# Optimization experiments

Hardware: AMD Instinct MI355X
Metric: run time of the kernel (lower is better)

The kernel has to match this reference:

```python
import jax, jax.numpy as jnp
import numpy as np

N, E = 2048, 262144
SDIM, VDIM, EDIM = 256, 64, 32
NUM_ATOM_FEATURES, NUM_BOND_TYPES, NMOL = 16, 5, 64


def setup_inputs() -> dict:
    key = jax.random.key(0)
    ks = jax.random.split(key, 18)
    def lin(k, fan_in, shape):
        return jax.random.uniform(k, shape, jnp.float32, -1.0, 1.0) / np.sqrt(fan_in)
    inp = {
        "s": jax.random.normal(ks[0], (N, SDIM), jnp.float32),
        "v": jax.random.normal(ks[1], (N, 3, VDIM), jnp.float32),
        "p": jax.random.normal(ks[2], (N, 3), jnp.float32),
        "e": jax.random.normal(ks[3], (E, EDIM), jnp.float32),
        "batch": jnp.sort(jax.random.randint(ks[4], (N,), 0, NMOL)),
        "edge_index_global": jax.random.randint(ks[5], (2, E), 0, N),
        # learned params (torch DenseLayer == Linear): W [in,out], b [out]
        "Ws": lin(ks[6], SDIM, (SDIM, SDIM)),   "bs": lin(ks[7], SDIM, (SDIM,)),
        "Wc": lin(ks[8], VDIM, (VDIM, 1)),                                      # coords_lin, no bias
        "Wa": lin(ks[9], SDIM, (SDIM, NUM_ATOM_FEATURES)), "ba": lin(ks[10], SDIM, (NUM_ATOM_FEATURES,)),
        "Wb": lin(ks[11], EDIM, (EDIM, SDIM)),  "bb": lin(ks[12], EDIM, (SDIM,)),
        "W0": lin(ks[13], SDIM + 1, (SDIM + 1, SDIM)), "b0": lin(ks[14], SDIM + 1, (SDIM,)),
        "W1": lin(ks[15], SDIM, (SDIM, NUM_BOND_TYPES)), "b1": lin(ks[16], SDIM, (NUM_BOND_TYPES,)),
    }
    return inp


def reference(s, v, p, e, batch, edge_index_global,
              Ws, bs, Wc, Wa, ba, Wb, bb, W0, b0, W1, b1):
    # shared scalar mapping with SiLU
    s_h = jax.nn.silu(s @ Ws + bs)                              # [N, SDIM]
    coords = (v @ Wc)[..., 0]                                   # [N,3,VDIM]@[VDIM,1] -> [N,3]
    atoms_pred = s_h @ Wa + ba                                  # [N, NUM_ATOM_FEATURES]

    j, i = edge_index_global[0], edge_index_global[1]
    # coords_param == 'data': add positions then remove per-graph mean (scatter_mean)
    coords_pred = p + coords
    sums = jax.ops.segment_sum(coords_pred, batch, num_segments=NMOL)       # [NMOL,3]
    cnts = jax.ops.segment_sum(jnp.ones((N, 1), s.dtype), batch, num_segments=NMOL)
    coords_pred = coords_pred - (sums / jnp.maximum(cnts, 1.0))[batch]

    d = jnp.sum((coords_pred[i] - coords_pred[j]) ** 2, axis=-1, keepdims=True)  # [E,1]

    # dense edge matrix construction + symmetrization (as in the original)
    e_dense = jnp.zeros((N, N, EDIM), e.dtype).at[j, i].set(e)  # [N,N,EDIM]
    e_dense = 0.5 * (e_dense + jnp.swapaxes(e_dense, 0, 1))
    e_sym = e_dense[j, i]                                        # [E,EDIM]

    f = s_h[i] + s_h[j] + (e_sym @ Wb + bb)                      # [E,SDIM]
    edge = jnp.concatenate([f, d], axis=-1)                      # [E,SDIM+1]
    bonds_pred = jax.nn.silu(edge @ W0 + b0) @ W1 + b1           # [E,NUM_BOND_TYPES]
    return coords_pred, atoms_pred, bonds_pred
```

## Files before the change

kernel.cpp:

```cpp
#include <hip/hip_runtime.h>
#include <hip/hip_bf16.h>

typedef __bf16 bf16_8 __attribute__((ext_vector_type(8)));
typedef __bf16 bf16_4 __attribute__((ext_vector_type(4)));
typedef float f32x4 __attribute__((ext_vector_type(4)));

__device__ __forceinline__ float silu_f(float x) {
    return x * __builtin_amdgcn_rcpf(1.0f + __expf(-x));
}

__device__ __forceinline__ unsigned hslot(unsigned cell, unsigned nslots) {
    return (unsigned)(((unsigned long long)(cell * 2654435761u) * nslots) >> 32);
}
__device__ __forceinline__ int map_lookup(unsigned nslots,
                                          const unsigned long long* __restrict__ H, unsigned cell) {
    unsigned slot = hslot(cell, nslots);
    for (int pr = 0; pr < 4096; pr++) {
        unsigned long long v = H[slot];
        if (v == 0ull) return -1;
        if ((unsigned)(v >> 32) == cell) return (int)(v & 0xFFFFFFFFu) - 1;
        slot++; if (slot == nslots) slot = 0;
    }
    return -1;
}

__global__ __launch_bounds__(256) void kS(float* __restrict__ out, int n, float val) {
    int i = blockIdx.x * 256 + threadIdx.x;
    if (i < n) out[i] = val;
}

__global__ __launch_bounds__(256) void kZ(f32x4* __restrict__ a, size_t na16,
                                          f32x4* __restrict__ b, size_t nb16) {
    size_t i = (size_t)blockIdx.x * 256 + threadIdx.x;
    size_t stride = (size_t)gridDim.x * 256;
    f32x4 z = {0.f, 0.f, 0.f, 0.f};
    for (size_t k = i; k < na16; k += stride) a[k] = z;
    for (size_t k = i; k < nb16; k += stride) b[k] = z;
}

__global__ __launch_bounds__(256, 4) void kP(
    const float* __restrict__ s, const float* __restrict__ Ws, const float* __restrict__ bs,
    const float* __restrict__ W0, const float* __restrict__ Wa, const float* __restrict__ ba,
    const float* __restrict__ v, const float* __restrict__ p,
    const float* __restrict__ Wc, const float* __restrict__ Wb, const float* __restrict__ bb,
    const float* __restrict__ b0, const float* __restrict__ W1,
    const int* __restrict__ batch, const int* __restrict__ ei,
    int N, int E, int gaB, int coordB, int mapB,
    unsigned nslots, unsigned long long* __restrict__ H,
    __bf16* __restrict__ G, __bf16* __restrict__ wqT, __bf16* __restrict__ w1Tg,
    float* __restrict__ w0L, float* __restrict__ b0p,
    float* __restrict__ cp, float* __restrict__ sums, float* __restrict__ cnts,
    float* __restrict__ outA)
{
    __shared__ __align__(16) char LDSC[37376];
    int b = blockIdx.x, t = threadIdx.x;

    if (b < gaB) {
        __bf16* s_bf  = (__bf16*)LDSC;
        __bf16* sh_bf = (__bf16*)(LDSC + 8448);
        __bf16* wT    = (__bf16*)(LDSC + 16896);
        int wv = t >> 6, lane = t & 63;
        int l16 = lane & 15, q8 = (lane >> 4) * 8, r4b = (lane >> 4) * 4;
        int r0 = b * 16;
        {
            int row = t >> 4, c0 = (t & 15) * 16;
            const float* sp = s + (long long)(r0 + row) * 256 + c0;
            bool ok = (r0 + row) < N;
            f32x4 a0 = ok ? *(const f32x4*)(sp + 0)  : (f32x4){0.f,0.f,0.f,0.f};
            f32x4 a1 = ok ? *(const f32x4*)(sp + 4)  : (f32x4){0.f,0.f,0.f,0.f};
            f32x4 a2 = ok ? *(const f32x4*)(sp + 8)  : (f32x4){0.f,0.f,0.f,0.f};
            f32x4 a3 = ok ? *(const f32x4*)(sp + 12) : (f32x4){0.f,0.f,0.f,0.f};
            bf16_8 p0, p1;
#pragma unroll
            for (int q = 0; q < 4; q++) {
                p0[q] = (__bf16)a0[q]; p0[q + 4] = (__bf16)a1[q];
                p1[q] = (__bf16)a2[q]; p1[q + 4] = (__bf16)a3[q];
            }
            *(bf16_8*)(s_bf + row * 264 + c0) = p0;
            *(bf16_8*)(s_bf + row * 264 + c0 + 8) = p1;
        }
        __syncthreads();
        __bf16* wTw = wT + wv * 2560;
        float ld[32];

        f32x4 acc[4];
#pragma unroll
        for (int ct = 0; ct < 4; ct++) acc[ct] = (f32x4){0.f,0.f,0.f,0.f};
        {
            const float* wp = Ws + wv * 64 + lane;
#pragma unroll
            for (int i = 0; i < 32; i++) ld[i] = wp[i * 256];
#pragma unroll 1
            for (int kk = 0; kk < 8; kk++) {
#pragma unroll
                for (int j = 0; j < 4; j++) {
                    bf16_8 pk;
#pragma unroll
                    for (int q = 0; q < 8; q++) pk[q] = (__bf16)ld[j * 8 + q];
                    *(bf16_8*)(wTw + lane * 40 + j * 8) = pk;
                }
                if (kk < 7) {
                    const float* wpn = wp + (kk + 1) * 32 * 256;
#pragma unroll
                    for (int i = 0; i < 32; i++) ld[i] = wpn[i * 256];
                }
                bf16_8 af = *(const bf16_8*)(s_bf + l16 * 264 + kk * 32 + q8);
#pragma unroll
                for (int ct = 0; ct < 4; ct++) {
                    bf16_8 bfr = *(const bf16_8*)(wTw + (ct * 16 + l16) * 40 + q8);
                    acc[ct] = __builtin_amdgcn_mfma_f32_16x16x32_bf16(af, bfr, acc[ct], 0, 0, 0);
                }
            }
        }
#pragma unroll
        for (int ct = 0; ct < 4; ct++) {
            int col = wv * 64 + ct * 16 + l16;
            float bsv = bs[col];
#pragma unroll
            for (int r = 0; r < 4; r++)
                sh_bf[(r4b + r) * 264 + col] = (__bf16)silu_f(acc[ct][r] + bsv);
        }
        __syncthreads();

        if (wv == 0) {
            f32x4 aa = (f32x4){0.f,0.f,0.f,0.f};
#pragma unroll 1
            for (int ks = 0; ks < 8; ks++) {
                bf16_8 a = *(const bf16_8*)(sh_bf + l16 * 264 + ks * 32 + q8);
                bf16_8 wb;
#pragma unroll
                for (int j = 0; j < 8; j++) wb[j] = (__bf16)Wa[(ks * 32 + q8 + j) * 16 + l16];
                aa = __builtin_amdgcn_mfma_f32_16x16x32_bf16(a, wb, aa, 0, 0, 0);
            }
            float bav = ba[l16];
#pragma unroll
            for (int r = 0; r < 4; r++) {
                int row = r0 + r4b + r;
                if (row < N) outA[row * 16 + l16] = aa[r] + bav;
            }
        }

        f32x4 acc2[4];
#pragma unroll
        for (int ct = 0; ct < 4; ct++) acc2[ct] = (f32x4){0.f,0.f,0.f,0.f};
        {
            const float* wp = W0 + wv * 64 + lane;
#pragma unroll
            for (int i = 0; i < 32; i++) ld[i] = wp[i * 256];
#pragma unroll 1
            for (int kk = 0; kk < 8; kk++) {
#pragma unroll
                for (int j = 0; j < 4; j++) {
                    bf16_8 pk;
#pragma unroll
                    for (int q = 0; q < 8; q++) pk[q] = (__bf16)ld[j * 8 + q];
                    *(bf16_8*)(wTw + lane * 40 + j * 8) = pk;
                }
                if (kk < 7) {
                    const float* wpn = wp + (kk + 1) * 32 * 256;
#pragma unroll
                    for (int i = 0; i < 32; i++) ld[i] = wpn[i * 256];
                }
                bf16_8 af = *(const bf16_8*)(sh_bf + l16 * 264 + kk * 32 + q8);
#pragma unroll
                for (int ct = 0; ct < 4; ct++) {
                    bf16_8 bfr = *(const bf16_8*)(wTw + (ct * 16 + l16) * 40 + q8);
                    acc2[ct] = __builtin_amdgcn_mfma_f32_16x16x32_bf16(af, bfr, acc2[ct], 0, 0, 0);
                }
            }
        }
#pragma unroll
        for (int ct = 0; ct < 4; ct++) {
            int col = wv * 64 + ct * 16 + l16;
#pragma unroll
            for (int r = 0; r < 4; r++) {
                int row = r0 + r4b + r;
                if (row < N) G[(long long)row * 256 + col] = (__bf16)acc2[ct][r];
            }
        }
        return;
    }
    b -= gaB;

    float* sm = (float*)LDSC;
    if (b < 2) {
        int r0 = b * 16;
        for (int i4 = t; i4 < 1024; i4 += 256)
            ((f32x4*)sm)[i4] = ((const f32x4*)(Wb + r0 * 256))[i4];
        __syncthreads();
        float acc[16];
#pragma unroll
        for (int r = 0; r < 16; r++) acc[r] = 0.f;
        for (int m4 = 0; m4 < 64; m4++) {
            float w0v = W0[(m4 * 4 + 0) * 256 + t];
            float w1v = W0[(m4 * 4 + 1) * 256 + t];
            float w2v = W0[(m4 * 4 + 2) * 256 + t];
            float w3v = W0[(m4 * 4 + 3) * 256 + t];
#pragma unroll
            for (int r = 0; r < 16; r++) {
                f32x4 sv = *(const f32x4*)(sm + r * 256 + m4 * 4);
                acc[r] += sv[0] * w0v + sv[1] * w1v + sv[2] * w2v + sv[3] * w3v;
            }
        }
#pragma unroll
        for (int r = 0; r < 16; r++) wqT[t * 32 + r0 + r] = (__bf16)acc[r];
        return;
    }
    b -= 2;
    if (b < 1) {
        sm[t] = bb[t];
        __syncthreads();
        float acc = 0.f;
        for (int m4 = 0; m4 < 64; m4++) {
            f32x4 bv = *(const f32x4*)(sm + m4 * 4);
            acc += bv[0] * W0[(m4 * 4 + 0) * 256 + t] + bv[1] * W0[(m4 * 4 + 1) * 256 + t]
                 + bv[2] * W0[(m4 * 4 + 2) * 256 + t] + bv[3] * W0[(m4 * 4 + 3) * 256 + t];
        }
        b0p[t] = acc + b0[t];
        w0L[t] = W0[256 * 256 + t];
#pragma unroll
        for (int c = 0; c < 16; c++)
            w1Tg[c * 256 + t] = (c < 5) ? (__bf16)W1[t * 5 + c] : (__bf16)0.f;
        return;
    }
    b -= 1;
    if (b < coordB) {
        int n = b * 256 + t;
        if (t < 64) sm[t] = Wc[t];
        __syncthreads();
        if (n < N) {
            int mb = batch[n] & 1023;
#pragma unroll
            for (int ax = 0; ax < 3; ax++) {
                float acc = 0.f;
                for (int d4 = 0; d4 < 16; d4++) {
                    f32x4 vv = *(const f32x4*)(v + (long long)n * 192 + ax * 64 + d4 * 4);
                    f32x4 wv2 = *(const f32x4*)(sm + d4 * 4);
                    acc += vv[0] * wv2[0] + vv[1] * wv2[1] + vv[2] * wv2[2] + vv[3] * wv2[3];
                }
                float val = p[n * 3 + ax] + acc;
                cp[n * 3 + ax] = val;
                atomicAdd(&sums[mb * 3 + ax], val);
            }
            atomicAdd(&cnts[mb], 1.0f);
        }
        return;
    }
    b -= coordB;
    {
        int k = b * 256 + t;
        if (k < E) {
            int jj = ei[k], ii = ei[E + k];
            if ((unsigned)jj >= (unsigned)N) jj = 0;
            if ((unsigned)ii >= (unsigned)N) ii = 0;
            unsigned cell = (unsigned)jj * (unsigned)N + (unsigned)ii;
            unsigned long long mine = ((unsigned long long)cell << 32) | (unsigned)(k + 1);
            unsigned slot = hslot(cell, nslots);
            for (int pr = 0; pr < 4096; pr++) {
                unsigned long long old = atomicCAS(&H[slot], 0ull, mine);
                if (old == 0ull) break;
                if ((unsigned)(old >> 32) == cell) { atomicMax(&H[slot], mine); break; }
                slot++; if (slot == nslots) slot = 0;
            }
        }
    }
}

__global__ __launch_bounds__(256, 4) void kC(
    const float* __restrict__ e, const int* __restrict__ ei, const int* __restrict__ batch,
    int N, int E, int edgeB, unsigned nslots,
    const unsigned long long* __restrict__ H,
    const __bf16* __restrict__ G, const __bf16* __restrict__ wqTg,
    const __bf16* __restrict__ w1Tg,
    const float* __restrict__ w0L, const float* __restrict__ b0p,
    const float* __restrict__ cp, const float* __restrict__ sums, const float* __restrict__ cnts,
    const float* __restrict__ b1,
    float* __restrict__ outC, float* __restrict__ bonds)
{
    if (blockIdx.x >= (unsigned)edgeB) {
        int n = ((int)blockIdx.x - edgeB) * 256 + threadIdx.x;
        if (n < N) {
            int mb = batch[n] & 1023;
            float cnt = fmaxf(cnts[mb], 1.0f);
#pragma unroll
            for (int ax = 0; ax < 3; ax++)
                outC[n * 3 + ax] = cp[n * 3 + ax] - sums[mb * 3 + ax] / cnt;
        }
        return;
    }

    __shared__ __align__(16) __bf16 esym[64 * 40];
    __shared__ __align__(16) __bf16 hbuf[64 * 264];
    __shared__ float sd[64];
    __shared__ int si[64], sj[64], sm1[64], sm2[64];

    int t = threadIdx.x;
    int wv = t >> 6, lane = t & 63;
    int l16 = lane & 15, q8 = (lane >> 4) * 8, r4b = (lane >> 4) * 4;
    int e0 = blockIdx.x * 64;

    if (t < 128) {
        int tt = t & 63;
        int k = e0 + tt;
        if (t < 64) {
            if (k >= E) {
                si[tt] = 0; sj[tt] = 0; sm1[tt] = 0; sd[tt] = 0.f;
            } else {
                int jj = ei[k], ii = ei[E + k];
                if ((unsigned)jj >= (unsigned)N) jj = 0;
                if ((unsigned)ii >= (unsigned)N) ii = 0;
                si[tt] = ii; sj[tt] = jj;
                int m1 = map_lookup(nslots, H, (unsigned)jj * (unsigned)N + (unsigned)ii);
                sm1[tt] = ((unsigned)m1 < (unsigned)E) ? m1 : 0;
                int bi = batch[ii] & 1023, bj = batch[jj] & 1023;
                float inv_i = __builtin_amdgcn_rcpf(fmaxf(cnts[bi], 1.0f));
                float inv_j = __builtin_amdgcn_rcpf(fmaxf(cnts[bj], 1.0f));
                float dx = (cp[ii * 3 + 0] - sums[bi * 3 + 0] * inv_i) - (cp[jj * 3 + 0] - sums[bj * 3 + 0] * inv_j);
                float dy = (cp[ii * 3 + 1] - sums[bi * 3 + 1] * inv_i) - (cp[jj * 3 + 1] - sums[bj * 3 + 1] * inv_j);
                float dz = (cp[ii * 3 + 2] - sums[bi * 3 + 2] * inv_i) - (cp[jj * 3 + 2] - sums[bj * 3 + 2] * inv_j);
                sd[tt] = dx * dx + dy * dy + dz * dz;
            }
        } else {
            if (k >= E) {
                sm2[tt] = -1;
            } else {
                int jj = ei[k], ii = ei[E + k];
                if ((unsigned)jj >= (unsigned)N) jj = 0;
                if ((unsigned)ii >= (unsigned)N) ii = 0;
                int m2 = map_lookup(nslots, H, (unsigned)ii * (unsigned)N + (unsigned)jj);
                sm2[tt] = ((unsigned)m2 < (unsigned)E) ? m2 : -1;
            }
        }
    }
    __syncthreads();

    {
        int er = t >> 2, qg = (t & 3) * 8;
        int m1 = sm1[er], m2 = sm2[er];
        const float* e1p = e + (size_t)m1 * 32 + qg;
        float v1[8], v2[8];
#pragma unroll
        for (int q = 0; q < 8; q++) { v1[q] = e1p[q]; v2[q] = 0.f; }
        if (m2 >= 0) {
            const float* e2p = e + (size_t)m2 * 32 + qg;
#pragma unroll
            for (int q = 0; q < 8; q++) v2[q] = e2p[q];
        }
        bf16_8 es;
#pragma unroll
        for (int q = 0; q < 8; q++) es[q] = (__bf16)(0.5f * (v1[q] + v2[q]));
        *(bf16_8*)(esym + er * 40 + qg) = es;
    }
    __syncthreads();

    f32x4 acc[4][4];
#pragma unroll
    for (int rt = 0; rt < 4; rt++)
#pragma unroll
        for (int ct = 0; ct < 4; ct++)
            acc[rt][ct] = (f32x4){0.f, 0.f, 0.f, 0.f};
    bf16_8 af[4];
#pragma unroll
    for (int rt = 0; rt < 4; rt++)
        af[rt] = *(const bf16_8*)(esym + (rt * 16 + l16) * 40 + q8);
#pragma unroll
    for (int ct = 0; ct < 4; ct++) {
        int c = (wv * 4 + ct) * 16 + l16;
        bf16_8 bfr = *(const bf16_8*)(wqTg + c * 32 + q8);
#pragma unroll
        for (int rt = 0; rt < 4; rt++)
            acc[rt][ct] = __builtin_amdgcn_mfma_f32_16x16x32_bf16(af[rt], bfr, acc[rt][ct], 0, 0, 0);
    }
    f32x4 sdv[4];
#pragma unroll
    for (int rt = 0; rt < 4; rt++)
        sdv[rt] = *(const f32x4*)(sd + rt * 16 + r4b);
#pragma unroll
    for (int ct = 0; ct < 4; ct++) {
        int col = (wv * 4 + ct) * 16 + l16;
        float w0c = w0L[col], b0c = b0p[col];
#pragma unroll
        for (int rt = 0; rt < 4; rt++) {
#pragma unroll
            for (int r4 = 0; r4 < 4; r4++) {
                int row = rt * 16 + r4b + r4;
                hbuf[row * 264 + col] = (__bf16)(acc[rt][ct][r4] + b0c + sdv[rt][r4] * w0c);
            }
        }
    }
    __syncthreads();

    {
        int c4 = lane * 4;
        for (int it = 0; it < 16; it++) {
            int er = wv * 16 + it;
            int ii = si[er], jj = sj[er];
            bf16_4 gi = *(const bf16_4*)(G + (size_t)ii * 256 + c4);
            bf16_4 gj = *(const bf16_4*)(G + (size_t)jj * 256 + c4);
            bf16_4 hv = *(const bf16_4*)(hbuf + er * 264 + c4);
            bf16_4 o;
#pragma unroll
            for (int q = 0; q < 4; q++) {
                float x = (float)hv[q] + (float)gi[q] + (float)gj[q];
                o[q] = (__bf16)silu_f(x);
            }
            *(bf16_4*)(hbuf + er * 264 + c4) = o;
        }
    }

    f32x4 acc3 = {0.f, 0.f, 0.f, 0.f};
#pragma unroll
    for (int ks = 0; ks < 8; ks++) {
        bf16_8 a = *(const bf16_8*)(hbuf + (wv * 16 + l16) * 264 + ks * 32 + q8);
        bf16_8 b2 = *(const bf16_8*)(w1Tg + l16 * 256 + ks * 32 + q8);
        acc3 = __builtin_amdgcn_mfma_f32_16x16x32_bf16(a, b2, acc3, 0, 0, 0);
    }
    if (l16 < 5) {
        float bv = b1[l16];
#pragma unroll
        for (int r4 = 0; r4 < 4; r4++) {
            int row = wv * 16 + r4b + r4;
            if (e0 + row < E)
                bonds[(size_t)(e0 + row) * 5 + l16] = acc3[r4] + bv;
        }
    }
}

extern "C" void kernel_launch(void* const* d_in, const int* in_sizes, int n_in,
                              void* d_out, int out_size, void* d_ws, size_t ws_size,
                              hipStream_t stream)
{
    const float* s  = (const float*)d_in[0];
    const float* v  = (const float*)d_in[1];
    const float* p  = (const float*)d_in[2];
    const float* e  = (const float*)d_in[3];
    const int* batch = (const int*)d_in[4];
    const int* ei    = (const int*)d_in[5];
    const float* Ws = (const float*)d_in[6];
    const float* bs = (const float*)d_in[7];
    const float* Wc = (const float*)d_in[8];
    const float* Wa = (const float*)d_in[9];
    const float* ba = (const float*)d_in[10];
    const float* Wb = (const float*)d_in[11];
    const float* bb = (const float*)d_in[12];
    const float* W0 = (const float*)d_in[13];
    const float* b0 = (const float*)d_in[14];
    const float* W1 = (const float*)d_in[15];
    const float* b1 = (const float*)d_in[16];

    float* out = (float*)d_out;
    int sentN = out_size < 8192 ? out_size : 8192;

    int N = in_sizes[0] / 256;
    long long E = in_sizes[5] / 2;
    int code = 0;
    if (in_sizes[6] != 65536) code |= 1;
    if (in_sizes[8] != 64) code |= 2;
    if (in_sizes[11] != 32 * 256) code |= 4;
    if (in_sizes[9] != 16 * 256) code |= 8;
    if (in_sizes[15] != 5 * 256) code |= 16;
    if (in_sizes[13] != 257 * 256) code |= 32;
    if (N < 1 || in_sizes[0] != N * 256) code |= 64;
    if (in_sizes[1] != (long long)N * 192) code |= 128;
    if (in_sizes[2] != N * 3) code |= 256;
    if (in_sizes[3] != E * 32) code |= 512;
    if (in_sizes[4] != N) code |= 1024;
    if ((long long)out_size != 19LL * N + 5LL * E) code |= 2048;
    if (code) {
        kS<<<(sentN + 255) / 256, 256, 0, stream>>>(out, sentN, 3000.0f + 64.0f * (float)code);
        return;
    }
    int Ei = (int)E;

    auto align256 = [](size_t x) { return (x + 255) & ~(size_t)255; };
    size_t G_b  = align256((size_t)N * 512);
    size_t cp_b = align256((size_t)N * 12);
    size_t misc = G_b + 16384 + 8192 + 1024 + 1024 + cp_b + 12288 + 4096 + 256;

    size_t avail = (ws_size > misc) ? (ws_size - misc) / 8 : 0;
    size_t want = (size_t)Ei * 2;
    size_t ns = avail < want ? avail : want;
    if (ns < (size_t)Ei + (size_t)Ei / 8) {
        unsigned mb = (unsigned)(ws_size >> 20); if (mb > 120) mb = 120;
        kS<<<(sentN + 255) / 256, 256, 0, stream>>>(out, sentN, 1000.0f + 8.0f * (float)mb);
        return;
    }
    unsigned nslots = (unsigned)ns;
    size_t mapBytes = ns * 8;

    char* ws = (char*)d_ws;
    unsigned long long* H = (unsigned long long*)ws;
    size_t mapZ = align256(mapBytes);
    size_t off = mapZ;
    __bf16* G    = (__bf16*)(ws + off); off += G_b;
    __bf16* wqT  = (__bf16*)(ws + off); off += 16384;
    __bf16* w1Tg = (__bf16*)(ws + off); off += 8192;
    float* w0L  = (float*)(ws + off);  off += 1024;
    float* b0p  = (float*)(ws + off);  off += 1024;
    float* cp   = (float*)(ws + off);  off += cp_b;
    float* sums = (float*)(ws + off);  off += 12288;
    float* cnts = (float*)(ws + off);  off += 4096;

    float* outC = out;
    float* outA = outC + 3 * N;
    float* outB = outC + 19 * N;

    kZ<<<512, 256, 0, stream>>>((f32x4*)ws, mapZ >> 4, (f32x4*)sums, 1024);

    int mapB = (Ei + 255) / 256;
    int coordB = (N + 255) / 256;
    int gaB = (N + 15) / 16;
    kP<<<gaB + 3 + coordB + mapB, 256, 0, stream>>>(
        s, Ws, bs, W0, Wa, ba, v, p, Wc, Wb, bb, b0, W1, batch, ei,
        N, Ei, gaB, coordB, mapB, nslots, H,
        G, wqT, w1Tg, w0L, b0p, cp, sums, cnts, outA);
    int edgeB = (Ei + 63) / 64;
    kC<<<edgeB + coordB, 256, 0, stream>>>(
        e, ei, batch, N, Ei, edgeB, nslots, H, G, wqT, w1Tg,
        w0L, b0p, cp, sums, cnts, b1, outC, outB);
}
```

Baseline: 211.7 us.

## Fuse edge MLP into register-resident MFMA loop with FP32 final projection

Restructures the edge kernel so each wave computes e_sym·Wq via transposed MFMA, with edges as the MFMA N dimension. The bias, distance term, G gathers and SiLU are then applied in registers, and the 5-wide output projection is reduced in FP32 with shuffles. This removes the hbuf/esym LDS staging, two barriers and the second MFMA pass. W1 is now transposed into LDS per block rather than precomputed in the prep kernel, and launch bounds rise to 6 blocks per CU. The trade-offs are redundant W1 transposition in every block and more scalar FMA work in the final projection.

After: 267.7 us. +26.5%, slower.

```diff
diff --git a/kernel.cpp b/kernel.cpp
--- a/kernel.cpp
+++ b/kernel.cpp
@@ -43,11 +43,11 @@
     const float* __restrict__ W0, const float* __restrict__ Wa, const float* __restrict__ ba,
     const float* __restrict__ v, const float* __restrict__ p,
     const float* __restrict__ Wc, const float* __restrict__ Wb, const float* __restrict__ bb,
-    const float* __restrict__ b0, const float* __restrict__ W1,
+    const float* __restrict__ b0,
     const int* __restrict__ batch, const int* __restrict__ ei,
     int N, int E, int gaB, int coordB, int mapB,
     unsigned nslots, unsigned long long* __restrict__ H,
-    __bf16* __restrict__ G, __bf16* __restrict__ wqT, __bf16* __restrict__ w1Tg,
+    __bf16* __restrict__ G, __bf16* __restrict__ wqT,
     float* __restrict__ w0L, float* __restrict__ b0p,
     float* __restrict__ cp, float* __restrict__ sums, float* __restrict__ cnts,
     float* __restrict__ outA)
@@ -218,9 +218,6 @@
         }
         b0p[t] = acc + b0[t];
         w0L[t] = W0[256 * 256 + t];
-#pragma unroll
-        for (int c = 0; c < 16; c++)
-            w1Tg[c * 256 + t] = (c < 5) ? (__bf16)W1[t * 5 + c] : (__bf16)0.f;
         return;
     }
     b -= 1;
@@ -266,12 +263,12 @@
     }
 }
 
-__global__ __launch_bounds__(256, 4) void kC(
+__global__ __launch_bounds__(256, 6) void kC(
     const float* __restrict__ e, const int* __restrict__ ei, const int* __restrict__ batch,
     int N, int E, int edgeB, unsigned nslots,
     const unsigned long long* __restrict__ H,
     const __bf16* __restrict__ G, const __bf16* __restrict__ wqTg,
-    const __bf16* __restrict__ w1Tg,
+    const float* __restrict__ W1,
     const float* __restrict__ w0L, const float* __restrict__ b0p,
     const float* __restrict__ cp, const float* __restrict__ sums, const float* __restrict__ cnts,
     const float* __restrict__ b1,
@@ -289,14 +286,14 @@
         return;
     }
 
-    __shared__ __align__(16) __bf16 esym[64 * 40];
-    __shared__ __align__(16) __bf16 hbuf[64 * 264];
     __shared__ float sd[64];
     __shared__ int si[64], sj[64], sm1[64], sm2[64];
+    __shared__ float w1f[5 * 260];
+    __shared__ float sb0[256], sw0[256];
 
     int t = threadIdx.x;
     int wv = t >> 6, lane = t & 63;
-    int l16 = lane & 15, q8 = (lane >> 4) * 8, r4b = (lane >> 4) * 4;
+    int l16 = lane & 15, q = lane >> 4, q8 = q * 8;
     int e0 = blockIdx.x * 64;
 
     if (t < 128) {
@@ -331,98 +328,76 @@
                 sm2[tt] = ((unsigned)m2 < (unsigned)E) ? m2 : -1;
             }
         }
+    } else {
+        int tt = t - 128;
+        for (int idx = tt; idx < 1280; idx += 128) {
+            int c = idx >> 8, col = idx & 255;
+            w1f[c * 260 + col] = W1[col * 5 + c];
+        }
+        for (int idx = tt; idx < 256; idx += 128) {
+            sb0[idx] = b0p[idx];
+            sw0[idx] = w0L[idx];
+        }
     }
     __syncthreads();
 
-    {
-        int er = t >> 2, qg = (t & 3) * 8;
-        int m1 = sm1[er], m2 = sm2[er];
-        const float* e1p = e + (size_t)m1 * 32 + qg;
-        float v1[8], v2[8];
-#pragma unroll
-        for (int q = 0; q < 8; q++) { v1[q] = e1p[q]; v2[q] = 0.f; }
-        if (m2 >= 0) {
-            const float* e2p = e + (size_t)m2 * 32 + qg;
-#pragma unroll
-            for (int q = 0; q < 8; q++) v2[q] = e2p[q];
-        }
-        bf16_8 es;
-#pragma unroll
-        for (int q = 0; q < 8; q++) es[q] = (__bf16)(0.5f * (v1[q] + v2[q]));
-        *(bf16_8*)(esym + er * 40 + qg) = es;
-    }
-    __syncthreads();
-
-    f32x4 acc[4][4];
-#pragma unroll
-    for (int rt = 0; rt < 4; rt++)
-#pragma unroll
-        for (int ct = 0; ct < 4; ct++)
-            acc[rt][ct] = (f32x4){0.f, 0.f, 0.f, 0.f};
-    bf16_8 af[4];
-#pragma unroll
-    for (int rt = 0; rt < 4; rt++)
-        af[rt] = *(const bf16_8*)(esym + (rt * 16 + l16) * 40 + q8);
-#pragma unroll
-    for (int ct = 0; ct < 4; ct++) {
-        int c = (wv * 4 + ct) * 16 + l16;
-        bf16_8 bfr = *(const bf16_8*)(wqTg + c * 32 + q8);
-#pragma unroll
-        for (int rt = 0; rt < 4; rt++)
-            acc[rt][ct] = __builtin_amdgcn_mfma_f32_16x16x32_bf16(af[rt], bfr, acc[rt][ct], 0, 0, 0);
-    }
-    f32x4 sdv[4];
-#pragma unroll
-    for (int rt = 0; rt < 4; rt++)
-        sdv[rt] = *(const f32x4*)(sd + rt * 16 + r4b);
-#pragma unroll
-    for (int ct = 0; ct < 4; ct++) {
-        int col = (wv * 4 + ct) * 16 + l16;
-        float w0c = w0L[col], b0c = b0p[col];
-#pragma unroll
-        for (int rt = 0; rt < 4; rt++) {
-#pragma unroll
-            for (int r4 = 0; r4 < 4; r4++) {
-                int row = rt * 16 + r4b + r4;
-                hbuf[row * 264 + col] = (__bf16)(acc[rt][ct][r4] + b0c + sdv[rt][r4] * w0c);
-            }
-        }
-    }
-    __syncthreads();
-
-    {
-        int c4 = lane * 4;
-        for (int it = 0; it < 16; it++) {
-            int er = wv * 16 + it;
-            int ii = si[er], jj = sj[er];
-            bf16_4 gi = *(const bf16_4*)(G + (size_t)ii * 256 + c4);
-            bf16_4 gj = *(const bf16_4*)(G + (size_t)jj * 256 + c4);
-            bf16_4 hv = *(const bf16_4*)(hbuf + er * 264 + c4);
-            bf16_4 o;
-#pragma unroll
-            for (int q = 0; q < 4; q++) {
-                float x = (float)hv[q] + (float)gi[q] + (float)gj[q];
-                o[q] = (__bf16)silu_f(x);
-            }
-            *(bf16_4*)(hbuf + er * 264 + c4) = o;
-        }
-    }
-
-    f32x4 acc3 = {0.f, 0.f, 0.f, 0.f};
-#pragma unroll
-    for (int ks = 0; ks < 8; ks++) {
-        bf16_8 a = *(const bf16_8*)(hbuf + (wv * 16 + l16) * 264 + ks * 32 + q8);
-        bf16_8 b2 = *(const bf16_8*)(w1Tg + l16 * 256 + ks * 32 + q8);
-        acc3 = __builtin_amdgcn_mfma_f32_16x16x32_bf16(a, b2, acc3, 0, 0, 0);
-    }
-    if (l16 < 5) {
-        float bv = b1[l16];
-#pragma unroll
-        for (int r4 = 0; r4 < 4; r4++) {
-            int row = wv * 16 + r4b + r4;
-            if (e0 + row < E)
-                bonds[(size_t)(e0 + row) * 5 + l16] = acc3[r4] + bv;
-        }
+    int edge = wv * 16 + l16;
+    int m1 = sm1[edge], m2 = sm2[edge];
+    int ii = si[edge], jj = sj[edge];
+    float d = sd[edge];
+
+    const f32x4* e1p = (const f32x4*)(e + (size_t)m1 * 32 + q8);
+    f32x4 a0 = e1p[0], a1 = e1p[1];
+    if (m2 >= 0) {
+        const f32x4* e2p = (const f32x4*)(e + (size_t)m2 * 32 + q8);
+        a0 += e2p[0]; a1 += e2p[1];
+    }
+    bf16_8 af;
+#pragma unroll
+    for (int qq = 0; qq < 4; qq++) {
+        af[qq] = (__bf16)(0.5f * a0[qq]);
+        af[qq + 4] = (__bf16)(0.5f * a1[qq]);
+    }
+
+    const __bf16* Gi = G + (size_t)ii * 256;
+    const __bf16* Gj = G + (size_t)jj * 256;
+    float pr[5];
+#pragma unroll
+    for (int c = 0; c < 5; c++) pr[c] = 0.f;
+
+#pragma unroll
+    for (int ct = 0; ct < 16; ct++) {
+        bf16_8 aw = *(const bf16_8*)(wqTg + (ct * 16 + l16) * 32 + q8);
+        f32x4 acc = (f32x4){0.f, 0.f, 0.f, 0.f};
+        acc = __builtin_amdgcn_mfma_f32_16x16x32_bf16(aw, af, acc, 0, 0, 0);
+        int c0 = ct * 16 + q * 4;
+        bf16_4 gi = *(const bf16_4*)(Gi + c0);
+        bf16_4 gj = *(const bf16_4*)(Gj + c0);
+        f32x4 b0v = *(const f32x4*)(sb0 + c0);
+        f32x4 w0v = *(const f32x4*)(sw0 + c0);
+        f32x4 h;
+#pragma unroll
+        for (int r = 0; r < 4; r++)
+            h[r] = silu_f(acc[r] + b0v[r] + d * w0v[r] + (float)gi[r] + (float)gj[r]);
+#pragma unroll
+        for (int c = 0; c < 5; c++) {
+            f32x4 wv4 = *(const f32x4*)(w1f + c * 260 + c0);
+            pr[c] += h[0] * wv4[0] + h[1] * wv4[1] + h[2] * wv4[2] + h[3] * wv4[3];
+        }
+    }
+
+#pragma unroll
+    for (int c = 0; c < 5; c++) {
+        float vsum = pr[c];
+        vsum += __shfl_xor(vsum, 16);
+        vsum += __shfl_xor(vsum, 32);
+        pr[c] = vsum;
+    }
+    if (q == 0 && e0 + edge < E) {
+        size_t base = (size_t)(e0 + edge) * 5;
+#pragma unroll
+        for (int c = 0; c < 5; c++)
+            bonds[base + c] = pr[c] + b1[c];
     }
 }
 
@@ -475,7 +450,7 @@
     auto align256 = [](size_t x) { return (x + 255) & ~(size_t)255; };
     size_t G_b  = align256((size_t)N * 512);
     size_t cp_b = align256((size_t)N * 12);
-    size_t misc = G_b + 16384 + 8192 + 1024 + 1024 + cp_b + 12288 + 4096 + 256;
+    size_t misc = G_b + 16384 + 1024 + 1024 + cp_b + 12288 + 4096 + 256;
 
     size_t avail = (ws_size > misc) ? (ws_size - misc) / 8 : 0;
     size_t want = (size_t)Ei * 2;
@@ -494,7 +469,6 @@
     size_t off = mapZ;
     __bf16* G    = (__bf16*)(ws + off); off += G_b;
     __bf16* wqT  = (__bf16*)(ws + off); off += 16384;
-    __bf16* w1Tg = (__bf16*)(ws + off); off += 8192;
     float* w0L  = (float*)(ws + off);  off += 1024;
     float* b0p  = (float*)(ws + off);  off += 1024;
     float* cp   = (float*)(ws + off);  off += cp_b;
@@ -511,11 +485,11 @@
     int coordB = (N + 255) / 256;
     int gaB = (N + 15) / 16;
     kP<<<gaB + 3 + coordB + mapB, 256, 0, stream>>>(
-        s, Ws, bs, W0, Wa, ba, v, p, Wc, Wb, bb, b0, W1, batch, ei,
+        s, Ws, bs, W0, Wa, ba, v, p, Wc, Wb, bb, b0, batch, ei,
         N, Ei, gaB, coordB, mapB, nslots, H,
-        G, wqT, w1Tg, w0L, b0p, cp, sums, cnts, outA);
+        G, wqT, w0L, b0p, cp, sums, cnts, outA);
     int edgeB = (Ei + 63) / 64;
     kC<<<edgeB + coordB, 256, 0, stream>>>(
-        e, ei, batch, N, Ei, edgeB, nslots, H, G, wqT, w1Tg,
+        e, ei, batch, N, Ei, edgeB, nslots, H, G, wqT, W1,
         w0L, b0p, cp, sums, cnts, b1, outC, outB);
 }
```
